# Optimization experiments

Measured on AMD Instinct MI355X. Metric: run time of the kernel, lower is better.

Reference implementation:

```python
import jax, jax.numpy as jnp
import numpy as np


def setup_inputs() -> dict:
    key = jax.random.key(0)
    ks = jax.random.split(key, 6)
    B, N, D, H, W = 8, 16, 128, 64, 64
    x = jax.random.normal(ks[0], (B, N, D, H, W), dtype=jnp.float32)
    mask = jax.random.randint(ks[1], (B, N, H, W), 0, 2, dtype=jnp.int32)
    s = 1.0 / np.sqrt(D)
    Wq = jax.random.normal(ks[2], (D, D), dtype=jnp.float32) * s
    bq = jax.random.normal(ks[3], (D,), dtype=jnp.float32) * s
    Wk = jax.random.normal(ks[4], (D, D), dtype=jnp.float32) * s
    bk = jax.random.normal(ks[5], (D,), dtype=jnp.float32) * s
    return {"x": x, "mask": mask, "Wq": Wq, "bq": bq, "Wk": Wk, "bk": bk}


def reference(x, mask, Wq, bq, Wk, bk):
    B, N, D, H, W = x.shape
    K = H * W
    # (B, N, K, D) token view of spatial grid
    xr = jnp.transpose(x, (0, 1, 3, 4, 2)).reshape(B, N, K, D)
    m = mask.reshape(B, N, K, 1).astype(x.dtype)
    valid_count = jnp.sum(m, axis=2, keepdims=True)          # (B, N, 1, 1)
    mean_x = jnp.sum(xr * m, axis=2, keepdims=True) / valid_count  # (B, N, 1, D)
    # Linear layers: y = x @ W^T + b (torch convention)
    query = mean_x @ Wq.T + bq                               # (B, N, 1, D)
    keys = xr @ Wk.T + bk                                    # (B, N, K, D)
    attn = jnp.einsum('bnqd,bnkd->bnqk', query, keys)        # (B, N, 1, K)
    neg_inf = jnp.array(-jnp.inf, dtype=attn.dtype)
    attn = jnp.where(m.reshape(B, N, 1, K) == 0, neg_inf, attn)
    attn = jax.nn.softmax(attn / jnp.sqrt(jnp.asarray(D, attn.dtype)), axis=-1)
    pooled = jnp.einsum('bnqk,bnkd->bnqd', attn, xr)         # (B, N, 1, D)
    return pooled[:, :, 0, :]                                 # (B, N, D)
```

## Files before the change

### kernel.cpp

```cpp
#include <hip/hip_runtime.h>
#include <math.h>

#define G 128
#define D 128
#define K 4096
#define CK 64

__global__ __launch_bounds__(256) void k1_mean(const float* __restrict__ x,
                                               const int* __restrict__ mask,
                                               float* __restrict__ meanacc,
                                               float* __restrict__ oacc,
                                               float* __restrict__ denomv) {
  const int g = blockIdx.x >> 5, s = blockIdx.x & 31;
  const int tid = threadIdx.x;
  if (s == 0) {
    if (tid < D) oacc[g * D + tid] = 0.0f;
    if (tid == D) denomv[g] = 0.0f;
  }
  const int wid = tid >> 6, lane = tid & 63;
  const int d = s * 4 + wid;
  const float4* x4 = (const float4*)(x + ((size_t)g * D + d) * K);
  const int4* m4 = (const int4*)(mask + (size_t)g * K);
  float4 acc = make_float4(0.f, 0.f, 0.f, 0.f);
#pragma unroll
  for (int it = 0; it < K / 256; ++it) {
    float4 a = x4[it * 64 + lane];
    int4 mi = m4[it * 64 + lane];
    acc.x += a.x * (float)mi.x;
    acc.y += a.y * (float)mi.y;
    acc.z += a.z * (float)mi.z;
    acc.w += a.w * (float)mi.w;
  }
  float sum = acc.x + acc.y + acc.z + acc.w;
#pragma unroll
  for (int o = 32; o > 0; o >>= 1) sum += __shfl_down(sum, o, 64);
  if (lane == 0) meanacc[g * D + d] = sum;
}

__global__ __launch_bounds__(128) void k2_query(
    const float* __restrict__ meanacc, const int* __restrict__ mask,
    const float* __restrict__ Wq, const float* __restrict__ bq,
    const float* __restrict__ Wk, const float* __restrict__ bk,
    float* __restrict__ qt, float* __restrict__ cvec) {
  __shared__ float mean_s[D], query_s[D], red[D];
  const int g = blockIdx.x, t = threadIdx.x;
  const int4* m4 = (const int4*)(mask + (size_t)g * K);
  int csum = 0;
  for (int i = t; i < K / 4; i += 128) {
    int4 v = m4[i];
    csum += v.x + v.y + v.z + v.w;
  }
  red[t] = (float)csum;
  __syncthreads();
  for (int o = 64; o > 0; o >>= 1) {
    if (t < o) red[t] += red[t + o];
    __syncthreads();
  }
  const float cnt = red[0];
  mean_s[t] = meanacc[g * D + t] / cnt;
  __syncthreads();
  float q = bq[t];
  for (int d = 0; d < D; ++d) q += mean_s[d] * Wq[t * D + d];
  query_s[t] = q;
  __syncthreads();
  red[t] = q * bk[t];
  __syncthreads();
  for (int o = 64; o > 0; o >>= 1) {
    if (t < o) red[t] += red[t + o];
    __syncthreads();
  }
  if (t == 0) cvec[g] = red[0];
  float qq = 0.f;
  for (int d = 0; d < D; ++d) qq += query_s[d] * Wk[d * D + t];
  qt[g * D + t] = qq;
}

__global__ __launch_bounds__(256) void k3_fused(
    const float* __restrict__ x, const int* __restrict__ mask,
    const float* __restrict__ qt, const float* __restrict__ cvec,
    float* __restrict__ oacc, float* __restrict__ denomv) {
  __shared__ float xs[D][CK + 1];
  __shared__ float part2[CK][17];
  __shared__ float wsm[CK];
  __shared__ float red[256];
  const int g = blockIdx.x >> 6;
  const int k0 = (blockIdx.x & 63) * CK;
  const int tid = threadIdx.x;
  const float4* xg = (const float4*)(x + (size_t)g * D * K + k0);
  const int j = tid & 15, owner = tid >> 4;
  float p0 = 0.f, p1 = 0.f, p2 = 0.f, p3 = 0.f;
#pragma unroll
  for (int it = 0; it < 8; ++it) {
    const int dd = owner + 16 * it;
    float4 v = xg[(size_t)dd * (K / 4) + j];
    float qv = qt[g * D + dd];
    xs[dd][4 * j + 0] = v.x;
    xs[dd][4 * j + 1] = v.y;
    xs[dd][4 * j + 2] = v.z;
    xs[dd][4 * j + 3] = v.w;
    p0 += qv * v.x;
    p1 += qv * v.y;
    p2 += qv * v.z;
    p3 += qv * v.w;
  }
  part2[4 * j + 0][owner] = p0;
  part2[4 * j + 1][owner] = p1;
  part2[4 * j + 2][owner] = p2;
  part2[4 * j + 3][owner] = p3;
  __syncthreads();
  if (tid < CK) {
    float l = 0.f;
#pragma unroll
    for (int o = 0; o < 16; ++o) l += part2[tid][o];
    const float scale = 0.08838834764831845f;
    l = (l + cvec[g]) * scale;
    float w = mask[(size_t)g * K + k0 + tid] ? __expf(l) : 0.f;
    wsm[tid] = w;
#pragma unroll
    for (int o = 32; o > 0; o >>= 1) w += __shfl_down(w, o, 64);
    if (tid == 0) atomicAdd(denomv + g, w);
  }
  __syncthreads();
  {
    const int dd = tid & 127, h = tid >> 7;
    float a2 = 0.f;
#pragma unroll 8
    for (int i = h * 32; i < h * 32 + 32; ++i) a2 += wsm[i] * xs[dd][i];
    red[tid] = a2;
  }
  __syncthreads();
  if (tid < D) atomicAdd(oacc + g * D + tid, red[tid] + red[tid + 128]);
}

__global__ __launch_bounds__(256) void k4_norm(const float* __restrict__ oacc,
                                               const float* __restrict__ denomv,
                                               float* __restrict__ out) {
  int i = blockIdx.x * 256 + threadIdx.x;
  out[i] = oacc[i] / denomv[i >> 7];
}

extern "C" void kernel_launch(void* const* d_in, const int* in_sizes, int n_in,
                              void* d_out, int out_size, void* d_ws,
                              size_t ws_size, hipStream_t stream) {
  const float* x = (const float*)d_in[0];
  const int* mask = (const int*)d_in[1];
  const float* Wq = (const float*)d_in[2];
  const float* bq = (const float*)d_in[3];
  const float* Wk = (const float*)d_in[4];
  const float* bk = (const float*)d_in[5];
  float* out = (float*)d_out;

  float* ws = (float*)d_ws;
  float* meanacc = ws;
  float* qt = ws + G * D;
  float* cvec = ws + 2 * G * D;
  float* oacc = ws + 2 * G * D + G;
  float* denomv = ws + 3 * G * D + G;

  k1_mean<<<G * 32, 256, 0, stream>>>(x, mask, meanacc, oacc, denomv);
  k2_query<<<G, 128, 0, stream>>>(meanacc, mask, Wq, bq, Wk, bk, qt, cvec);
  k3_fused<<<G * (K / CK), 256, 0, stream>>>(x, mask, qt, cvec, oacc, denomv);
  k4_norm<<<(G * D) / 256, 256, 0, stream>>>(oacc, denomv, out);
}
```

Measured before the change: 436.3 us.

## Keep x tile in registers in fused kernel and vectorize query projection

```diff
diff --git a/kernel.cpp b/kernel.cpp
--- a/kernel.cpp
+++ b/kernel.cpp
@@ -42,7 +42,8 @@
     const float* __restrict__ Wq, const float* __restrict__ bq,
     const float* __restrict__ Wk, const float* __restrict__ bk,
     float* __restrict__ qt, float* __restrict__ cvec) {
-  __shared__ float mean_s[D], query_s[D], red[D];
+  __shared__ __align__(16) float mean_s[D];
+  __shared__ float query_s[D], red[D];
   const int g = blockIdx.x, t = threadIdx.x;
   const int4* m4 = (const int4*)(mask + (size_t)g * K);
   int csum = 0;
@@ -60,7 +61,15 @@
   mean_s[t] = meanacc[g * D + t] / cnt;
   __syncthreads();
   float q = bq[t];
-  for (int d = 0; d < D; ++d) q += mean_s[d] * Wq[t * D + d];
+  {
+    const float4* wq4 = (const float4*)(Wq + (size_t)t * D);
+    const float4* ms4 = (const float4*)mean_s;
+#pragma unroll
+    for (int dc = 0; dc < D / 4; ++dc) {
+      float4 w = wq4[dc], m = ms4[dc];
+      q += w.x * m.x + w.y * m.y + w.z * m.z + w.w * m.w;
+    }
+  }
   query_s[t] = q;
   __syncthreads();
   red[t] = q * bk[t];
@@ -71,6 +80,7 @@
   }
   if (t == 0) cvec[g] = red[0];
   float qq = 0.f;
+#pragma unroll 8
   for (int d = 0; d < D; ++d) qq += query_s[d] * Wk[d * D + t];
   qt[g * D + t] = qq;
 }
@@ -79,29 +89,26 @@
     const float* __restrict__ x, const int* __restrict__ mask,
     const float* __restrict__ qt, const float* __restrict__ cvec,
     float* __restrict__ oacc, float* __restrict__ denomv) {
-  __shared__ float xs[D][CK + 1];
   __shared__ float part2[CK][17];
-  __shared__ float wsm[CK];
-  __shared__ float red[256];
-  const int g = blockIdx.x >> 6;
+  __shared__ __align__(16) float wsm[CK];
+  __shared__ __align__(16) float part3[D][20];
+  const int g = (G - 1) - (int)(blockIdx.x >> 6);
   const int k0 = (blockIdx.x & 63) * CK;
   const int tid = threadIdx.x;
+  const int j = tid & 15, owner = tid >> 4;
   const float4* xg = (const float4*)(x + (size_t)g * D * K + k0);
-  const int j = tid & 15, owner = tid >> 4;
+  const float* qtg = qt + g * D;
+  float4 v[8];
   float p0 = 0.f, p1 = 0.f, p2 = 0.f, p3 = 0.f;
 #pragma unroll
   for (int it = 0; it < 8; ++it) {
     const int dd = owner + 16 * it;
-    float4 v = xg[(size_t)dd * (K / 4) + j];
-    float qv = qt[g * D + dd];
-    xs[dd][4 * j + 0] = v.x;
-    xs[dd][4 * j + 1] = v.y;
-    xs[dd][4 * j + 2] = v.z;
-    xs[dd][4 * j + 3] = v.w;
-    p0 += qv * v.x;
-    p1 += qv * v.y;
-    p2 += qv * v.z;
-    p3 += qv * v.w;
+    v[it] = xg[(size_t)dd * (K / 4) + j];
+    const float qv = qtg[dd];
+    p0 += qv * v[it].x;
+    p1 += qv * v[it].y;
+    p2 += qv * v[it].z;
+    p3 += qv * v[it].w;
   }
   part2[4 * j + 0][owner] = p0;
   part2[4 * j + 1][owner] = p1;
@@ -122,14 +129,22 @@
   }
   __syncthreads();
   {
-    const int dd = tid & 127, h = tid >> 7;
-    float a2 = 0.f;
-#pragma unroll 8
-    for (int i = h * 32; i < h * 32 + 32; ++i) a2 += wsm[i] * xs[dd][i];
-    red[tid] = a2;
+    const float4 wv = *(const float4*)&wsm[4 * j];
+#pragma unroll
+    for (int it = 0; it < 8; ++it) {
+      const int dd = owner + 16 * it;
+      part3[dd][j] =
+          wv.x * v[it].x + wv.y * v[it].y + wv.z * v[it].z + wv.w * v[it].w;
+    }
   }
   __syncthreads();
-  if (tid < D) atomicAdd(oacc + g * D + tid, red[tid] + red[tid + 128]);
+  if (tid < D) {
+    const float4* r4 = (const float4*)part3[tid];
+    float4 a = r4[0], b = r4[1], c = r4[2], e = r4[3];
+    float o = a.x + a.y + a.z + a.w + b.x + b.y + b.z + b.w + c.x + c.y + c.z +
+              c.w + e.x + e.y + e.z + e.w;
+    atomicAdd(oacc + g * D + tid, o);
+  }
 }
 
 __global__ __launch_bounds__(256) void k4_norm(const float* __restrict__ oacc,
```

New measurement: 433.2 us. No clear change (-0.7%).
